# Performance work log

Hardware: AMD Instinct MI355X
Metric: run time of the kernel (lower is better)

The kernel has to match this reference:

```python
import jax, jax.numpy as jnp
import numpy as np

WEIGHT = 1e-7
SIGMA_RGB = 15.0
SIGMA_XY = 100.0
SCALE = 0.5


def _nearest_resize(x, Ho, Wo):
    # torch F.interpolate mode='nearest': src = floor(dst * in/out)
    H, W = x.shape[-2], x.shape[-1]
    iy = (jnp.arange(Ho) * (H / Ho)).astype(jnp.int32)
    ix = (jnp.arange(Wo) * (W / Wo)).astype(jnp.int32)
    return x[..., iy[:, None], ix[None, :]]


def _bilinear_resize(x, Ho, Wo):
    # torch bilinear, align_corners=False (half-pixel centers, no antialias)
    H, W = x.shape[-2], x.shape[-1]
    yc = jnp.clip((jnp.arange(Ho, dtype=jnp.float32) + 0.5) * (H / Ho) - 0.5, 0.0, H - 1.0)
    xc = jnp.clip((jnp.arange(Wo, dtype=jnp.float32) + 0.5) * (W / Wo) - 0.5, 0.0, W - 1.0)
    y0 = jnp.floor(yc).astype(jnp.int32); y1 = jnp.minimum(y0 + 1, H - 1); ty = yc - y0
    x0 = jnp.floor(xc).astype(jnp.int32); x1 = jnp.minimum(x0 + 1, W - 1); tx = xc - x0
    g = lambda yi, xi: x[..., yi[:, None], xi[None, :]]
    top = g(y0, x0) * (1.0 - tx) + g(y0, x1) * tx
    bot = g(y1, x0) * (1.0 - tx) + g(y1, x1) * tx
    return top * (1.0 - ty[:, None]) + bot * ty[:, None]


def _dense_energy(images, segmentations, ROIs, seg_label):
    N, K, H, W = segmentations.shape
    Ho, Wo = int(H * SCALE), int(W * SCALE)
    P = Ho * Wo
    img_s = _nearest_resize(images, Ho, Wo)            # [N,3,Ho,Wo]
    seg_s = _bilinear_resize(segmentations, Ho, Wo)    # [N,K,Ho,Wo]
    roi_s = _nearest_resize(ROIs, Ho, Wo)              # [N,Ho,Wo]
    lbl_s = _nearest_resize(seg_label, Ho, Wo)         # [N,1,Ho,Wo]
    unlabel = (lbl_s == 255)[:, 0]                     # [N,Ho,Wo]

    # Gate = clamp(ROI - max_k seg, min=0), with unlabeled region forced to 1
    gate = roi_s - jnp.max(seg_s, axis=1)
    gate = jnp.where(unlabel, 1.0, gate)
    gate = jnp.maximum(gate, 0.0)
    gate = jax.lax.stop_gradient(gate)                 # constant in the custom backward

    seg_roi = seg_s * roi_s[:, None]                   # [N,K,Ho,Wo]

    sxy = SIGMA_XY * SCALE
    yy, xx = jnp.meshgrid(jnp.arange(Ho, dtype=jnp.float32),
                          jnp.arange(Wo, dtype=jnp.float32), indexing='ij')
    pos = jnp.stack([xx.ravel() / sxy, yy.ravel() / sxy], axis=-1)  # [P,2]

    def per_image(img, seg):
        # img [3,Ho,Wo], seg [K,Ho,Wo] -> AS [K,P]: Gaussian bilateral filter
        col = img.reshape(img.shape[0], P).T / SIGMA_RGB            # [P,3]
        f = jnp.concatenate([pos, col], axis=-1)                    # [P,5]
        sq = jnp.sum(f * f, axis=-1)
        d2 = jnp.maximum(sq[:, None] + sq[None, :] - 2.0 * (f @ f.T), 0.0)
        Wm = jnp.exp(-0.5 * d2)                                     # [P,P] affinity
        return seg.reshape(seg.shape[0], P) @ Wm                    # symmetric Wm

    AS = jax.vmap(per_image)(img_s, seg_roi)                        # [N,K,P]
    AS = AS * gate.reshape(N, 1, P)
    loss = -jnp.sum(seg_roi.reshape(N, K, P) * AS) / N
    return (WEIGHT * loss).reshape(1)


def setup_inputs() -> dict:
    key = jax.random.key(0)
    k1, k2, k3, k4 = jax.random.split(key, 4)
    N, C, K, H, W = 4, 3, 21, 128, 128
    images = jax.random.uniform(k1, (N, C, H, W), dtype=jnp.float32) * 255.0
    segmentations = jax.nn.softmax(jax.random.normal(k2, (N, K, H, W), dtype=jnp.float32), axis=1)
    ROIs = jax.random.randint(k3, (N, H, W), 0, 2).astype(jnp.float32)
    seg_label = jax.random.randint(k4, (N, 1, H, W), 0, 256).astype(jnp.int32)
    return {"images": images, "segmentations": segmentations, "ROIs": ROIs, "seg_label": seg_label}


def reference(images, segmentations, ROIs, seg_label):
    return _dense_energy(images, segmentations, ROIs, seg_label)
```

## Files before the change

kernel.cpp:

```cpp
#include <hip/hip_runtime.h>
#include <hip/hip_bf16.h>


typedef _Float16 v8h __attribute__((ext_vector_type(8)));
typedef float v16f __attribute__((ext_vector_type(16)));

#define NIMG 4
#define KCH 21
#define HIN 128
#define WIN 128
#define PPX 4096
#define TPB 32
#define TRI 528
#define NBLK (NIMG * TRI)

#define WS_S_OFF 0x000000
#define WS_F_OFF 0x180000
#define PART_OFF 0x200000
#define CNT_OFF  0x202100

#define SQRT_LOG2E 1.2011224087864498f

__device__ __forceinline__ float fexp2(float x) {
#if __has_builtin(__builtin_amdgcn_exp2f)
    return __builtin_amdgcn_exp2f(x);
#else
    return __expf(x * 0.69314718055994531f);
#endif
}

__global__ __launch_bounds__(256) void prep_kernel(
    const float* __restrict__ img, const float* __restrict__ seg,
    const float* __restrict__ roi, const int* __restrict__ lbl,
    char* __restrict__ ws)
{
    __shared__ int gexcl[256];
    __shared__ unsigned gflags[256];
    __shared__ int wsum[4];

    int n  = blockIdx.x >> 4;
    int bl = blockIdx.x & 15;
    int t  = threadIdx.x;

    {
        int sy = t >> 2, sx0 = (t & 3) * 16;
        const float* srow = roi + ((size_t)n * HIN + 2 * sy) * WIN + 2 * sx0;
        unsigned flags = 0; int cl = 0;
        #pragma unroll
        for (int v = 0; v < 8; v++) {
            float4 q = *(const float4*)(srow + 4 * v);
            if (q.x != 0.f) { flags |= 1u << (2 * v);     cl++; }
            if (q.z != 0.f) { flags |= 1u << (2 * v + 1); cl++; }
        }
        int lane = t & 63, wv = t >> 6;
        int v = cl;
        #pragma unroll
        for (int off = 1; off < 64; off <<= 1) {
            int u = __shfl_up(v, off, 64);
            if (lane >= off) v += u;
        }
        if (lane == 63) wsum[wv] = v;
        __syncthreads();
        int base = 0;
        #pragma unroll
        for (int k = 0; k < 4; k++) if (k < wv) base += wsum[k];
        gexcl[t] = base + v - cl;
        gflags[t] = flags;
        __syncthreads();
    }
    int total = wsum[0] + wsum[1] + wsum[2] + wsum[3];

    int p = bl * 256 + t;
    int g = p >> 4, o = p & 15;
    unsigned f = gflags[g];
    bool active = (f >> o) & 1u;
    int slot_in = gexcl[g] + __popc(f & ((1u << o) - 1u));

    if (bl == 0 && t == 0) ((int*)(ws + CNT_OFF))[n] = total;

    if (bl == 15) {
        int padEnd = (total + 127) & ~127;
        if (padEnd > PPX) padEnd = PPX;
        const float4 z4 = make_float4(0.f, 0.f, 0.f, 0.f);
        int s = total + t;
        if (s < padEnd) {
            float4* dS = (float4*)(ws + WS_S_OFF + ((size_t)n * PPX + s) * 96);
            #pragma unroll
            for (int u = 0; u < 6; u++) dS[u] = z4;
            float4* dF = (float4*)(ws + WS_F_OFF + ((size_t)n * PPX + s) * 32);
            dF[0] = z4; dF[1] = z4;
        }
    }

    if (!active) return;
    int slot = (n << 12) | slot_in;

    int y = p >> 6, x = p & 63, iy = 2 * y, ix = 2 * x;
    const float inv_rgb = SQRT_LOG2E / 15.0f, inv_sxy = SQRT_LOG2E / 50.0f;

    int lb = lbl[((size_t)n * HIN + iy) * WIN + ix];

    float sv[KCH]; float maxs = 0.0f;
    #pragma unroll
    for (int k = 0; k < KCH; k++) {
        const float* sp = seg + ((((size_t)n * KCH + k) * HIN + iy) * WIN + ix);
        float2 a = *(const float2*)sp;
        float2 c = *(const float2*)(sp + WIN);
        float s = 0.25f * (a.x + a.y + c.x + c.y);
        maxs = fmaxf(maxs, s);
        sv[k] = s;
    }
    float gate = (lb == 255) ? 1.0f : fmaxf(1.0f - maxs, 0.0f);

    union { float4 q[6]; _Float16 e[48]; } rs;
    #pragma unroll
    for (int k = 0; k < KCH; k++) {
        rs.e[k] = (_Float16)(sv[k] * gate);
        rs.e[24 + k] = (_Float16)sv[k];
    }
    #pragma unroll
    for (int k = KCH; k < 24; k++) { rs.e[k] = (_Float16)0.f; rs.e[24 + k] = (_Float16)0.f; }

    float fv[5];
    fv[0] = (float)x * inv_sxy;
    fv[1] = (float)y * inv_sxy;
    fv[2] = img[(((size_t)n * 3 + 0) * HIN + iy) * WIN + ix] * inv_rgb;
    fv[3] = img[(((size_t)n * 3 + 1) * HIN + iy) * WIN + ix] * inv_rgb;
    fv[4] = img[(((size_t)n * 3 + 2) * HIN + iy) * WIN + ix] * inv_rgb;

    _Float16 hi[5], lo[5];
    float sq = 0.f;
    #pragma unroll
    for (int u = 0; u < 5; u++) {
        hi[u] = (_Float16)fv[u];
        lo[u] = (_Float16)(fv[u] - (float)hi[u]);
        float fe = (float)hi[u] + (float)lo[u];
        sq = fmaf(fe, fe, sq);
    }
    float sqv = -0.5f * sq;
    _Float16 sqh = (_Float16)sqv;
    _Float16 sql = (_Float16)(sqv - (float)sqh);
    const _Float16 h0 = (_Float16)0.f, h1 = (_Float16)1.f;

    union { float4 q[2]; _Float16 e[16]; } rf;
    #pragma unroll
    for (int u = 0; u < 5; u++) { rf.e[u] = hi[u]; rf.e[8 + u] = lo[u]; }
    rf.e[5] = sqh; rf.e[6] = sql; rf.e[7] = h1;
    rf.e[13] = h0; rf.e[14] = h0; rf.e[15] = h1;

    float4* ds = (float4*)(ws + WS_S_OFF + (size_t)slot * 96);
    #pragma unroll
    for (int u = 0; u < 6; u++) ds[u] = rs.q[u];
    float4* df = (float4*)(ws + WS_F_OFF + (size_t)slot * 32);
    df[0] = rf.q[0]; df[1] = rf.q[1];
}

#define LSTR 104
#define FSTR 40
#define SREG_O 0
#define FREG_O 26624
#define RED_O  36864
#define LDS_BYTES 36880

__global__ __launch_bounds__(256)
__attribute__((amdgpu_waves_per_eu(1, 4)))
void pairs_kernel(
    const char* __restrict__ ws, float* __restrict__ part)
{
    __shared__ __align__(16) char smem[LDS_BYTES];
    int b = blockIdx.x;
    int n = b / TRI, r = b - n * TRI;
    int i = 0, rowlen = TPB;
    while (r >= rowlen) { r -= rowlen; rowlen--; i++; }
    int j = i + r;
    bool diag = (i == j);

    int cnt = ((const int*)(ws + CNT_OFF))[n];
    int Tn = (cnt + 127) >> 7;
    if (j >= Tn) {
        if (threadIdx.x == 0) part[b] = 0.f;
        return;
    }

    int t = threadIdx.x;
    int lane = t & 63, half = lane >> 5, lr = lane & 31, wv = t >> 6;
    int wq = wv & 1, wp = wv >> 1;

    {
        const float4* gsi = (const float4*)(ws + WS_S_OFF) + (size_t)(n * PPX + i * 128) * 6;
        #pragma unroll
        for (int k = 0; k < 3; k++) {
            int v = t + k * 256;
            int row = v / 6, off = v - row * 6;
            float4 vs = gsi[v];
            char* dS = smem + SREG_O + row * LSTR + off * 16;
            *(float2*)dS = make_float2(vs.x, vs.y);
            *(float2*)(dS + 8) = make_float2(vs.z, vs.w);
        }
        const float4* gfi = (const float4*)(ws + WS_F_OFF) + (size_t)(n * PPX + i * 128) * 2;
        {
            int row = t >> 1, off = t & 1;
            float4 vf = gfi[t];
            char* dF = smem + FREG_O + row * FSTR + off * 16;
            *(float2*)dF = make_float2(vf.x, vf.y);
            *(float2*)(dF + 8) = make_float2(vf.z, vf.w);
        }
        if (!diag) {
            const float4* gsj = (const float4*)(ws + WS_S_OFF) + (size_t)(n * PPX + j * 128) * 6;
            #pragma unroll
            for (int k = 0; k < 3; k++) {
                int v = t + k * 256;
                int row = v / 6, off = v - row * 6;
                float4 vs = gsj[v];
                char* dS = smem + SREG_O + (128 + row) * LSTR + off * 16;
                *(float2*)dS = make_float2(vs.x, vs.y);
                *(float2*)(dS + 8) = make_float2(vs.z, vs.w);
            }
            const float4* gfj = (const float4*)(ws + WS_F_OFF) + (size_t)(n * PPX + j * 128) * 2;
            int row = t >> 1, off = t & 1;
            float4 vf = gfj[t];
            char* dF = smem + FREG_O + (128 + row) * FSTR + off * 16;
            *(float2*)dF = make_float2(vf.x, vf.y);
            *(float2*)(dF + 8) = make_float2(vf.z, vf.w);
        }
    }
    __syncthreads();

    int jrow0 = diag ? 0 : 128;
    const _Float16 selA = half ? (_Float16)0.f : (_Float16)1.f;
    float ac0 = 0.f, ac1 = 0.f, ac2 = 0.f, ac3 = 0.f;

    #pragma unroll
    for (int sp = 0; sp < 2; sp++) {
        int pr = wp * 64 + sp * 32 + lr;
        const char* sb = smem + SREG_O + pr * LSTR;
        const char* fb = smem + FREG_O + pr * FSTR;
        union { v8h h; float2 f[2]; } A0, A1, A2, Af;
        A0.f[0] = *(const float2*)(sb + half * 16);
        A0.f[1] = *(const float2*)(sb + half * 16 + 8);
        A1.f[0] = *(const float2*)(sb + 32 + half * 16);
        A1.f[1] = *(const float2*)(sb + 32 + half * 16 + 8);
        A2.f[0] = *(const float2*)(sb + 64 + half * 16);
        A2.f[1] = *(const float2*)(sb + 64 + half * 16 + 8);
        Af.f[0] = *(const float2*)(fb + half * 16);
        Af.f[1] = *(const float2*)(fb + half * 16 + 8);

        #pragma unroll
        for (int s = 0; s < 2; s++) {
            int cr = jrow0 + wq * 64 + s * 32 + lr;
            const char* cb = smem + SREG_O + cr * LSTR;
            const char* gb = smem + FREG_O + cr * FSTR;
            union { v8h h; float2 f[2]; } B0, B1, B2;
            union { v8h h; float2 f[2]; _Float16 e[8]; } U, L;
            B0.f[0] = *(const float2*)(cb + 48 + half * 16);
            B0.f[1] = *(const float2*)(cb + 48 + half * 16 + 8);
            int o1 = half ? 0 : 80;
            B1.f[0] = *(const float2*)(cb + o1);
            B1.f[1] = *(const float2*)(cb + o1 + 8);
            B2.f[0] = *(const float2*)(cb + 16 + half * 16);
            B2.f[1] = *(const float2*)(cb + 16 + half * 16 + 8);
            U.f[0] = *(const float2*)(gb);      U.f[1] = *(const float2*)(gb + 8);
            L.f[0] = *(const float2*)(gb + 16); L.f[1] = *(const float2*)(gb + 24);

            union { v8h h; _Float16 e[8]; } Bf1, Bf2;
            Bf1.h = U.h;
            Bf1.e[5] = selA; Bf1.e[6] = selA;
            Bf1.e[7] = half ? U.e[6] : U.e[5];
            Bf2.h = L.h;
            Bf2.e[7] = (_Float16)0.f;

            v16f z = {0.f,0.f,0.f,0.f,0.f,0.f,0.f,0.f,0.f,0.f,0.f,0.f,0.f,0.f,0.f,0.f};
            v16f c2 = __builtin_amdgcn_mfma_f32_32x32x16_f16(Af.h, Bf1.h, z, 0, 0, 0);
            c2 = __builtin_amdgcn_mfma_f32_32x32x16_f16(Af.h, Bf2.h, c2, 0, 0, 0);
            v16f c1 = __builtin_amdgcn_mfma_f32_32x32x16_f16(A0.h, B0.h, z, 0, 0, 0);
            c1 = __builtin_amdgcn_mfma_f32_32x32x16_f16(A1.h, B1.h, c1, 0, 0, 0);
            c1 = __builtin_amdgcn_mfma_f32_32x32x16_f16(A2.h, B2.h, c1, 0, 0, 0);

            #pragma unroll
            for (int rr = 0; rr < 16; rr++) {
                float arg = fminf(c2[rr], 0.0f);
                float w = fexp2(arg);
                if ((rr & 3) == 0)      ac0 = fmaf(w, c1[rr], ac0);
                else if ((rr & 3) == 1) ac1 = fmaf(w, c1[rr], ac1);
                else if ((rr & 3) == 2) ac2 = fmaf(w, c1[rr], ac2);
                else                    ac3 = fmaf(w, c1[rr], ac3);
            }
        }
    }

    float acc = (ac0 + ac1) + (ac2 + ac3);
    #pragma unroll
    for (int off = 32; off > 0; off >>= 1) acc += __shfl_down(acc, off, 64);
    float* wred = (float*)(smem + RED_O);
    if ((t & 63) == 0) wred[t >> 6] = acc;
    __syncthreads();
    if (t == 0) {
        float partial = (wred[0] + wred[1]) + (wred[2] + wred[3]);
        if (diag) partial *= 0.5f;
        part[b] = partial;
    }
}

__global__ __launch_bounds__(256) void finalize_kernel(
    const float* __restrict__ part, float* __restrict__ out)
{
    __shared__ float s[256];
    int t = threadIdx.x;
    float v = 0.f;
    #pragma unroll
    for (int k = 0; k < 9; k++) {
        int idx = t + k * 256;
        if (idx < NBLK) v += part[idx];
    }
    s[t] = v;
    __syncthreads();
    #pragma unroll
    for (int off = 128; off > 0; off >>= 1) {
        if (t < off) s[t] += s[t + off];
        __syncthreads();
    }
    if (t == 0) out[0] = s[0] * (-1e-7f / (float)NIMG);
}

extern "C" void kernel_launch(void* const* d_in, const int* in_sizes, int n_in,
                              void* d_out, int out_size, void* d_ws, size_t ws_size,
                              hipStream_t stream) {
    const float* images = (const float*)d_in[0];
    const float* seg    = (const float*)d_in[1];
    const float* rois   = (const float*)d_in[2];
    const int*   lbl    = (const int*)d_in[3];
    float* out = (float*)d_out;
    char*  ws  = (char*)d_ws;
    float* part = (float*)(ws + PART_OFF);

    hipLaunchKernelGGL(prep_kernel, dim3((NIMG * PPX) / 256), dim3(256), 0, stream,
                       images, seg, rois, lbl, ws);
    hipLaunchKernelGGL(pairs_kernel, dim3(NBLK), dim3(256), 0, stream,
                       (const char*)ws, part);
    hipLaunchKernelGGL(finalize_kernel, dim3(1), dim3(256), 0, stream,
                       (const float*)part, out);
}
```

Before: 77.02 us.

## Fuse prep into pairs kernel, recomputing compaction and features per block

Removes the separate prep kernel and its workspace round-trip. Each pairs block now redoes the ROI prefix-sum compaction for its image, maps its two 128-slot tiles back to pixels, and computes the half-precision seg and feature rows directly into LDS from the raw inputs. This saves one kernel launch and the global write and read of the packed features. In exchange every block repeats the ROI scan and the seg gathers, which adds redundant global reads and work. The block-to-tile mapping also changes to a j-major triangular order.

Measured after the change: 89.51 us. 1.16x slower.

```diff
diff --git a/kernel.cpp b/kernel.cpp
--- a/kernel.cpp
+++ b/kernel.cpp
@@ -14,10 +14,7 @@
 #define TRI 528
 #define NBLK (NIMG * TRI)
 
-#define WS_S_OFF 0x000000
-#define WS_F_OFF 0x180000
-#define PART_OFF 0x200000
-#define CNT_OFF  0x202100
+#define PART_OFF 0x000000
 
 #define SQRT_LOG2E 1.2011224087864498f
 
@@ -29,203 +26,161 @@
 #endif
 }
 
-__global__ __launch_bounds__(256) void prep_kernel(
+#define LSTR 104
+#define FSTR 40
+#define SREG_O 0
+#define FREG_O 26624
+#define RED_O  36864
+#define SLOT_O 36880
+#define WSUM_O 37392
+#define LDS_BYTES 37408
+
+__global__ __launch_bounds__(256)
+__attribute__((amdgpu_waves_per_eu(1, 4)))
+void pairs_kernel(
     const float* __restrict__ img, const float* __restrict__ seg,
     const float* __restrict__ roi, const int* __restrict__ lbl,
-    char* __restrict__ ws)
+    float* __restrict__ part)
 {
-    __shared__ int gexcl[256];
-    __shared__ unsigned gflags[256];
-    __shared__ int wsum[4];
-
-    int n  = blockIdx.x >> 4;
-    int bl = blockIdx.x & 15;
-    int t  = threadIdx.x;
-
+    __shared__ __align__(16) char smem[LDS_BYTES];
+    unsigned short* slotpix = (unsigned short*)(smem + SLOT_O);
+    int* wsum = (int*)(smem + WSUM_O);
+
+    int b = blockIdx.x;
+    int n = b / TRI, r = b - n * TRI;
+    int j = 0;
+    while (r > j) { r -= j + 1; j++; }
+    int i = r;
+    bool diag = (i == j);
+
+    int t = threadIdx.x;
+    int lane = t & 63, wv = t >> 6;
+
+    slotpix[t] = 0xFFFFu;
+    unsigned flags = 0; int cl = 0;
     {
         int sy = t >> 2, sx0 = (t & 3) * 16;
         const float* srow = roi + ((size_t)n * HIN + 2 * sy) * WIN + 2 * sx0;
-        unsigned flags = 0; int cl = 0;
         #pragma unroll
         for (int v = 0; v < 8; v++) {
             float4 q = *(const float4*)(srow + 4 * v);
             if (q.x != 0.f) { flags |= 1u << (2 * v);     cl++; }
             if (q.z != 0.f) { flags |= 1u << (2 * v + 1); cl++; }
         }
-        int lane = t & 63, wv = t >> 6;
-        int v = cl;
+    }
+    int v = cl;
+    #pragma unroll
+    for (int off = 1; off < 64; off <<= 1) {
+        int u = __shfl_up(v, off, 64);
+        if (lane >= off) v += u;
+    }
+    if (lane == 63) wsum[wv] = v;
+    __syncthreads();
+    int base = 0;
+    #pragma unroll
+    for (int k = 0; k < 4; k++) if (k < wv) base += wsum[k];
+    int excl  = base + v - cl;
+    int total = wsum[0] + wsum[1] + wsum[2] + wsum[3];
+
+    int Tn = (total + 127) >> 7;
+    if (j >= Tn) {
+        if (t == 0) part[b] = 0.f;
+        return;
+    }
+
+    {
+        int i128 = i << 7, j128 = j << 7;
+        int s = excl;
         #pragma unroll
-        for (int off = 1; off < 64; off <<= 1) {
-            int u = __shfl_up(v, off, 64);
-            if (lane >= off) v += u;
-        }
-        if (lane == 63) wsum[wv] = v;
-        __syncthreads();
-        int base = 0;
-        #pragma unroll
-        for (int k = 0; k < 4; k++) if (k < wv) base += wsum[k];
-        gexcl[t] = base + v - cl;
-        gflags[t] = flags;
-        __syncthreads();
-    }
-    int total = wsum[0] + wsum[1] + wsum[2] + wsum[3];
-
-    int p = bl * 256 + t;
-    int g = p >> 4, o = p & 15;
-    unsigned f = gflags[g];
-    bool active = (f >> o) & 1u;
-    int slot_in = gexcl[g] + __popc(f & ((1u << o) - 1u));
-
-    if (bl == 0 && t == 0) ((int*)(ws + CNT_OFF))[n] = total;
-
-    if (bl == 15) {
-        int padEnd = (total + 127) & ~127;
-        if (padEnd > PPX) padEnd = PPX;
-        const float4 z4 = make_float4(0.f, 0.f, 0.f, 0.f);
-        int s = total + t;
-        if (s < padEnd) {
-            float4* dS = (float4*)(ws + WS_S_OFF + ((size_t)n * PPX + s) * 96);
-            #pragma unroll
-            for (int u = 0; u < 6; u++) dS[u] = z4;
-            float4* dF = (float4*)(ws + WS_F_OFF + ((size_t)n * PPX + s) * 32);
-            dF[0] = z4; dF[1] = z4;
-        }
-    }
-
-    if (!active) return;
-    int slot = (n << 12) | slot_in;
-
-    int y = p >> 6, x = p & 63, iy = 2 * y, ix = 2 * x;
-    const float inv_rgb = SQRT_LOG2E / 15.0f, inv_sxy = SQRT_LOG2E / 50.0f;
-
-    int lb = lbl[((size_t)n * HIN + iy) * WIN + ix];
-
-    float sv[KCH]; float maxs = 0.0f;
-    #pragma unroll
-    for (int k = 0; k < KCH; k++) {
-        const float* sp = seg + ((((size_t)n * KCH + k) * HIN + iy) * WIN + ix);
-        float2 a = *(const float2*)sp;
-        float2 c = *(const float2*)(sp + WIN);
-        float s = 0.25f * (a.x + a.y + c.x + c.y);
-        maxs = fmaxf(maxs, s);
-        sv[k] = s;
-    }
-    float gate = (lb == 255) ? 1.0f : fmaxf(1.0f - maxs, 0.0f);
-
-    union { float4 q[6]; _Float16 e[48]; } rs;
-    #pragma unroll
-    for (int k = 0; k < KCH; k++) {
-        rs.e[k] = (_Float16)(sv[k] * gate);
-        rs.e[24 + k] = (_Float16)sv[k];
-    }
-    #pragma unroll
-    for (int k = KCH; k < 24; k++) { rs.e[k] = (_Float16)0.f; rs.e[24 + k] = (_Float16)0.f; }
-
-    float fv[5];
-    fv[0] = (float)x * inv_sxy;
-    fv[1] = (float)y * inv_sxy;
-    fv[2] = img[(((size_t)n * 3 + 0) * HIN + iy) * WIN + ix] * inv_rgb;
-    fv[3] = img[(((size_t)n * 3 + 1) * HIN + iy) * WIN + ix] * inv_rgb;
-    fv[4] = img[(((size_t)n * 3 + 2) * HIN + iy) * WIN + ix] * inv_rgb;
-
-    _Float16 hi[5], lo[5];
-    float sq = 0.f;
-    #pragma unroll
-    for (int u = 0; u < 5; u++) {
-        hi[u] = (_Float16)fv[u];
-        lo[u] = (_Float16)(fv[u] - (float)hi[u]);
-        float fe = (float)hi[u] + (float)lo[u];
-        sq = fmaf(fe, fe, sq);
-    }
-    float sqv = -0.5f * sq;
-    _Float16 sqh = (_Float16)sqv;
-    _Float16 sql = (_Float16)(sqv - (float)sqh);
-    const _Float16 h0 = (_Float16)0.f, h1 = (_Float16)1.f;
-
-    union { float4 q[2]; _Float16 e[16]; } rf;
-    #pragma unroll
-    for (int u = 0; u < 5; u++) { rf.e[u] = hi[u]; rf.e[8 + u] = lo[u]; }
-    rf.e[5] = sqh; rf.e[6] = sql; rf.e[7] = h1;
-    rf.e[13] = h0; rf.e[14] = h0; rf.e[15] = h1;
-
-    float4* ds = (float4*)(ws + WS_S_OFF + (size_t)slot * 96);
-    #pragma unroll
-    for (int u = 0; u < 6; u++) ds[u] = rs.q[u];
-    float4* df = (float4*)(ws + WS_F_OFF + (size_t)slot * 32);
-    df[0] = rf.q[0]; df[1] = rf.q[1];
-}
-
-#define LSTR 104
-#define FSTR 40
-#define SREG_O 0
-#define FREG_O 26624
-#define RED_O  36864
-#define LDS_BYTES 36880
-
-__global__ __launch_bounds__(256)
-__attribute__((amdgpu_waves_per_eu(1, 4)))
-void pairs_kernel(
-    const char* __restrict__ ws, float* __restrict__ part)
-{
-    __shared__ __align__(16) char smem[LDS_BYTES];
-    int b = blockIdx.x;
-    int n = b / TRI, r = b - n * TRI;
-    int i = 0, rowlen = TPB;
-    while (r >= rowlen) { r -= rowlen; rowlen--; i++; }
-    int j = i + r;
-    bool diag = (i == j);
-
-    int cnt = ((const int*)(ws + CNT_OFF))[n];
-    int Tn = (cnt + 127) >> 7;
-    if (j >= Tn) {
-        if (threadIdx.x == 0) part[b] = 0.f;
-        return;
-    }
-
-    int t = threadIdx.x;
-    int lane = t & 63, half = lane >> 5, lr = lane & 31, wv = t >> 6;
+        for (int u = 0; u < 16; u++) {
+            if ((flags >> u) & 1u) {
+                int p = t * 16 + u;
+                int d = s - i128;
+                if ((unsigned)d < 128u) slotpix[d] = (unsigned short)p;
+                if (!diag) {
+                    int e = s - j128;
+                    if ((unsigned)e < 128u) slotpix[128 + e] = (unsigned short)p;
+                }
+                s++;
+            }
+        }
+    }
+    __syncthreads();
+
+    if (!diag || t < 128) {
+        int pix = slotpix[t];
+        float2* dS = (float2*)(smem + SREG_O + t * LSTR);
+        float2* dF = (float2*)(smem + FREG_O + t * FSTR);
+        if (pix == 0xFFFFu) {
+            const float2 z2 = make_float2(0.f, 0.f);
+            #pragma unroll
+            for (int u = 0; u < 12; u++) dS[u] = z2;
+            #pragma unroll
+            for (int u = 0; u < 4; u++) dF[u] = z2;
+        } else {
+            int y = pix >> 6, x = pix & 63, iy = 2 * y, ix = 2 * x;
+            const float inv_rgb = SQRT_LOG2E / 15.0f, inv_sxy = SQRT_LOG2E / 50.0f;
+
+            int lb = lbl[((size_t)n * HIN + iy) * WIN + ix];
+
+            float sv[KCH]; float maxs = 0.0f;
+            #pragma unroll
+            for (int k = 0; k < KCH; k++) {
+                const float* sp = seg + ((((size_t)n * KCH + k) * HIN + iy) * WIN + ix);
+                float2 a = *(const float2*)sp;
+                float2 c = *(const float2*)(sp + WIN);
+                float s = 0.25f * (a.x + a.y + c.x + c.y);
+                maxs = fmaxf(maxs, s);
+                sv[k] = s;
+            }
+            float gate = (lb == 255) ? 1.0f : fmaxf(1.0f - maxs, 0.0f);
+
+            union { float2 d[12]; _Float16 e[48]; } rs;
+            #pragma unroll
+            for (int k = 0; k < KCH; k++) {
+                rs.e[k] = (_Float16)(sv[k] * gate);
+                rs.e[24 + k] = (_Float16)sv[k];
+            }
+            #pragma unroll
+            for (int k = KCH; k < 24; k++) { rs.e[k] = (_Float16)0.f; rs.e[24 + k] = (_Float16)0.f; }
+
+            float fv[5];
+            fv[0] = (float)x * inv_sxy;
+            fv[1] = (float)y * inv_sxy;
+            fv[2] = img[(((size_t)n * 3 + 0) * HIN + iy) * WIN + ix] * inv_rgb;
+            fv[3] = img[(((size_t)n * 3 + 1) * HIN + iy) * WIN + ix] * inv_rgb;
+            fv[4] = img[(((size_t)n * 3 + 2) * HIN + iy) * WIN + ix] * inv_rgb;
+
+            _Float16 hi[5], lo[5];
+            float sq = 0.f;
+            #pragma unroll
+            for (int u = 0; u < 5; u++) {
+                hi[u] = (_Float16)fv[u];
+                lo[u] = (_Float16)(fv[u] - (float)hi[u]);
+                float fe = (float)hi[u] + (float)lo[u];
+                sq = fmaf(fe, fe, sq);
+            }
+            float sqv = -0.5f * sq;
+            _Float16 sqh = (_Float16)sqv;
+            _Float16 sql = (_Float16)(sqv - (float)sqh);
+            const _Float16 h0 = (_Float16)0.f, h1 = (_Float16)1.f;
+
+            union { float2 d[4]; _Float16 e[16]; } rf;
+            #pragma unroll
+            for (int u = 0; u < 5; u++) { rf.e[u] = hi[u]; rf.e[8 + u] = lo[u]; }
+            rf.e[5] = sqh; rf.e[6] = sql; rf.e[7] = h1;
+            rf.e[13] = h0; rf.e[14] = h0; rf.e[15] = h1;
+
+            #pragma unroll
+            for (int u = 0; u < 12; u++) dS[u] = rs.d[u];
+            #pragma unroll
+            for (int u = 0; u < 4; u++) dF[u] = rf.d[u];
+        }
+    }
+    __syncthreads();
+
+    int half = lane >> 5, lr = lane & 31;
     int wq = wv & 1, wp = wv >> 1;
-
-    {
-        const float4* gsi = (const float4*)(ws + WS_S_OFF) + (size_t)(n * PPX + i * 128) * 6;
-        #pragma unroll
-        for (int k = 0; k < 3; k++) {
-            int v = t + k * 256;
-            int row = v / 6, off = v - row * 6;
-            float4 vs = gsi[v];
-            char* dS = smem + SREG_O + row * LSTR + off * 16;
-            *(float2*)dS = make_float2(vs.x, vs.y);
-            *(float2*)(dS + 8) = make_float2(vs.z, vs.w);
-        }
-        const float4* gfi = (const float4*)(ws + WS_F_OFF) + (size_t)(n * PPX + i * 128) * 2;
-        {
-            int row = t >> 1, off = t & 1;
-            float4 vf = gfi[t];
-            char* dF = smem + FREG_O + row * FSTR + off * 16;
-            *(float2*)dF = make_float2(vf.x, vf.y);
-            *(float2*)(dF + 8) = make_float2(vf.z, vf.w);
-        }
-        if (!diag) {
-            const float4* gsj = (const float4*)(ws + WS_S_OFF) + (size_t)(n * PPX + j * 128) * 6;
-            #pragma unroll
-            for (int k = 0; k < 3; k++) {
-                int v = t + k * 256;
-                int row = v / 6, off = v - row * 6;
-                float4 vs = gsj[v];
-                char* dS = smem + SREG_O + (128 + row) * LSTR + off * 16;
-                *(float2*)dS = make_float2(vs.x, vs.y);
-                *(float2*)(dS + 8) = make_float2(vs.z, vs.w);
-            }
-            const float4* gfj = (const float4*)(ws + WS_F_OFF) + (size_t)(n * PPX + j * 128) * 2;
-            int row = t >> 1, off = t & 1;
-            float4 vf = gfj[t];
-            char* dF = smem + FREG_O + (128 + row) * FSTR + off * 16;
-            *(float2*)dF = make_float2(vf.x, vf.y);
-            *(float2*)(dF + 8) = make_float2(vf.z, vf.w);
-        }
-    }
-    __syncthreads();
-
     int jrow0 = diag ? 0 : 128;
     const _Float16 selA = half ? (_Float16)0.f : (_Float16)1.f;
     float ac0 = 0.f, ac1 = 0.f, ac2 = 0.f, ac3 = 0.f;
@@ -333,10 +288,8 @@
     char*  ws  = (char*)d_ws;
     float* part = (float*)(ws + PART_OFF);
 
-    hipLaunchKernelGGL(prep_kernel, dim3((NIMG * PPX) / 256), dim3(256), 0, stream,
-                       images, seg, rois, lbl, ws);
     hipLaunchKernelGGL(pairs_kernel, dim3(NBLK), dim3(256), 0, stream,
-                       (const char*)ws, part);
+                       images, seg, rois, lbl, part);
     hipLaunchKernelGGL(finalize_kernel, dim3(1), dim3(256), 0, stream,
                        (const float*)part, out);
 }
```
